# Optimization experiments

Hardware: AMD Instinct MI355X
Metric: run time of the kernel (lower is better)

Reference implementation:

```python
import jax, jax.numpy as jnp
import numpy as np

N = 65536   # nodes
D = 128     # in_dim == emb_dim (required by GRUCell usage)
E = 524288  # edges, pre-sorted by topological level
L = 8       # number of topological levels (edge_masks)


def _gru(x, h, Wi, Wh, bi, bh):
    # torch.nn.GRUCell semantics
    gi = x @ Wi.T + bi            # [*, 3D]
    gh = h @ Wh.T + bh
    ir, iz, i_n = jnp.split(gi, 3, axis=-1)
    hr, hz, h_n = jnp.split(gh, 3, axis=-1)
    r = jax.nn.sigmoid(ir + hr)
    z = jax.nn.sigmoid(iz + hz)
    n = jnp.tanh(i_n + r * h_n)
    return (1.0 - z) * n + z * h


def _direction(h_prev, j_lev, i_lev, ea_lev, We, be, Wa, ba, Wi, Wh, bi, bh):
    # j = message source (h_j gathered), i = aggregation target (segment index)
    n_nodes = h_prev.shape[0]
    # roots = nodes never appearing as aggregation target -> GRU with zero hidden
    root = ~jnp.zeros((n_nodes,), bool).at[i_lev.reshape(-1)].set(True)
    h = jnp.where(root[:, None], _gru(h_prev, jnp.zeros_like(h_prev), Wi, Wh, bi, bh), 0.0)

    def step(h, lev):
        j, i, ea = lev                       # [El], [El], [El, D]
        e = ea @ We.T + be                   # edge_lin
        q = h_prev[i]                        # h_prev_i
        k = h[j] + e                         # h_j + edge_emb
        v = h[j]
        alpha = (jnp.concatenate([q, k], axis=-1) @ Wa.T + ba)[:, 0]  # [El]
        # segment softmax over aggregation index i (numerically stable)
        m = jax.lax.stop_gradient(jax.ops.segment_max(alpha, i, num_segments=n_nodes))
        ex = jnp.exp(alpha - m[i])
        den = jax.ops.segment_sum(ex, i, num_segments=n_nodes)
        a = ex / den[i]
        msg = jax.ops.segment_sum(a[:, None] * v, i, num_segments=n_nodes)  # [N, D]
        mask = jnp.zeros((n_nodes,), bool).at[i].set(True)
        h_new = _gru(h_prev, msg, Wi, Wh, bi, bh)
        return jnp.where(mask[:, None], h_new, h), None

    h, _ = jax.lax.scan(step, h, (j_lev, i_lev, ea_lev))
    return h


def setup_inputs() -> dict:
    key = jax.random.key(0)
    ks = jax.random.split(key, 24)
    p = lambda k, shape: (0.05 * jax.random.normal(k, shape)).astype(jnp.float32)
    inp = {
        'x': jax.random.normal(ks[0], (N, D), jnp.float32),
        'edge_index': jax.random.randint(ks[1], (2, E), 0, N, dtype=jnp.int32),
        'edge_attr': jax.random.normal(ks[2], (E, D), jnp.float32),
        'num_levels': L,
        # forward-direction AttnConv + GRUCell params
        'We_f': p(ks[3], (D, D)), 'be_f': p(ks[4], (D,)),
        'Wa_f': p(ks[5], (1, 2 * D)), 'ba_f': p(ks[6], (1,)),
        'Wi_f': p(ks[7], (3 * D, D)), 'Wh_f': p(ks[8], (3 * D, D)),
        'bi_f': p(ks[9], (3 * D,)), 'bh_f': p(ks[10], (3 * D,)),
        # backward-direction params
        'We_b': p(ks[11], (D, D)), 'be_b': p(ks[12], (D,)),
        'Wa_b': p(ks[13], (1, 2 * D)), 'ba_b': p(ks[14], (1,)),
        'Wi_b': p(ks[15], (3 * D, D)), 'Wh_b': p(ks[16], (3 * D, D)),
        'bi_b': p(ks[17], (3 * D,)), 'bh_b': p(ks[18], (3 * D,)),
    }
    return inp


def reference(x, edge_index, edge_attr, num_levels,
              We_f, be_f, Wa_f, ba_f, Wi_f, Wh_f, bi_f, bh_f,
              We_b, be_b, Wa_b, ba_b, Wi_b, Wh_b, bi_b, bh_b):
    El = edge_index.shape[1] // num_levels
    src = edge_index[0].reshape(num_levels, El)
    dst = edge_index[1].reshape(num_levels, El)
    ea = edge_attr.reshape(num_levels, El, -1)
    # forward pass over levels: flow source->target, aggregate at dst
    h_fwd = _direction(x, src, dst, ea, We_f, be_f, Wa_f, ba_f, Wi_f, Wh_f, bi_f, bh_f)
    # fnb: backward pass takes h_fwd as h_prev; flow target->source (aggregate at src),
    # levels iterated in reverse
    h_bwd = _direction(h_fwd, dst[::-1], src[::-1], ea[::-1],
                       We_b, be_b, Wa_b, ba_b, Wi_b, Wh_b, bi_b, bh_b)
    return jax.nn.relu(h_bwd)
```

## Files before the change

### kernel.cpp

```cpp
#include <hip/hip_runtime.h>
#include <cstdint>
#include <cstddef>

constexpr int N_NODES = 65536;
constexpr int D       = 128;
constexpr int E_EDGES = 524288;
constexpr int LVLS    = 8;
constexpr int EL      = E_EDGES / LVLS;
constexpr int OSTR    = 65540;
constexpr int WIMG_M  = 131072;

typedef unsigned int  u32;
typedef unsigned short u16;
typedef __attribute__((ext_vector_type(8)))  short short8;
typedef __attribute__((ext_vector_type(16))) float f32x16;

__device__ __forceinline__ float sigmoidf_(float x) { return 1.0f / (1.0f + expf(-x)); }

__device__ __forceinline__ u32 bf_hi(float f) {
    u32 x = __float_as_uint(f);
    return (x + 0x7fffu + ((x >> 16) & 1u)) >> 16;
}
__device__ __forceinline__ float bf_f(u32 hbits) { return __uint_as_float(hbits << 16); }

__device__ __forceinline__ int swz(int row, int kbyte) {
    return row * 64 + (kbyte ^ ((row & 3) << 4));
}

__device__ __forceinline__ void gload_lds16(const void* g, void* l) {
    __builtin_amdgcn_global_load_lds(
        (const __attribute__((address_space(1))) unsigned int*)g,
        (__attribute__((address_space(3))) unsigned int*)l, 16, 0, 0);
}

__device__ __forceinline__ float wave_sum(float v) {
#pragma unroll
    for (int off = 32; off > 0; off >>= 1) v += __shfl_down(v, off, 64);
    return v;
}

__global__ __launch_bounds__(256)
void prep_kernel(const float* __restrict__ We_f, const float* __restrict__ Wa_f,
                 const float* __restrict__ be_f, const float* __restrict__ ba_f,
                 const float* __restrict__ We_b, const float* __restrict__ Wa_b,
                 const float* __restrict__ be_b, const float* __restrict__ ba_b,
                 float* __restrict__ u_f, float* __restrict__ u_b, float* __restrict__ cst)
{
    int t = threadIdx.x;
    if (t < 128) {
        float s = 0.f;
        for (int d = 0; d < 128; ++d) s = fmaf(We_f[d * 128 + t], Wa_f[128 + d], s);
        u_f[t] = s;
    } else {
        int c = t - 128;
        float s = 0.f;
        for (int d = 0; d < 128; ++d) s = fmaf(We_b[d * 128 + c], Wa_b[128 + d], s);
        u_b[c] = s;
    }
    if (t == 0) {
        float s = 0.f;
        for (int d = 0; d < 128; ++d) s = fmaf(be_f[d], Wa_f[128 + d], s);
        cst[0] = s + ba_f[0];
    }
    if (t == 255) {
        float s = 0.f;
        for (int d = 0; d < 128; ++d) s = fmaf(be_b[d], Wa_b[128 + d], s);
        cst[1] = s + ba_b[0];
    }
}

__global__ __launch_bounds__(256)
void convert_w4(const float* __restrict__ W0, const float* __restrict__ W1,
                const float* __restrict__ W2, const float* __restrict__ W3,
                unsigned char* __restrict__ img)
{
    const float* Ws[4] = {W0, W1, W2, W3};
    int m = blockIdx.y;
    int i = blockIdx.x * 256 + threadIdx.x;
    int rw = i >> 7, k = i & 127;
    float v = Ws[m][i];
    u32 hb = bf_hi(v);
    u32 lb = bf_hi(v - bf_f(hb));
    int ks = k >> 5, kb = (k & 31) * 2;
    size_t base = (size_t)m * WIMG_M + (size_t)ks * 32768;
    *reinterpret_cast<u16*>(img + base + swz(rw, kb)) = (u16)hb;
    if (rw >= 256)
        *reinterpret_cast<u16*>(img + base + 24576 + swz(rw - 256, kb)) = (u16)lb;
}

__global__ __launch_bounds__(256)
void edot_kernel(const float* __restrict__ ea, const float* __restrict__ u_f,
                 const float* __restrict__ u_b, const float* __restrict__ cst,
                 float* __restrict__ edot_f, float* __restrict__ edot_b)
{
    int wv = threadIdx.x >> 6, lane = threadIdx.x & 63;
    int e = blockIdx.x * 4 + wv;
    if (e >= E_EDGES) return;
    int d = lane << 1;
    float2 v  = *reinterpret_cast<const float2*>(ea + (size_t)e * 128 + d);
    float2 uf = *reinterpret_cast<const float2*>(u_f + d);
    float2 ub = *reinterpret_cast<const float2*>(u_b + d);
    float af = wave_sum(v.x * uf.x + v.y * uf.y);
    float ab = wave_sum(v.x * ub.x + v.y * ub.y);
    if (lane == 0) {
        edot_f[e] = af + cst[0];
        edot_b[e] = ab + cst[1];
    }
}

__global__ __launch_bounds__(256)
void count_flags(const int* __restrict__ ei, int* __restrict__ counts,
                 int* __restrict__ flag_f, int* __restrict__ flag_b)
{
    int e = blockIdx.x * 256 + threadIdx.x;
    int lv = e >> 16;
    int s = ei[e], t = ei[E_EDGES + e];
    atomicAdd(&counts[(size_t)lv * 65536 + t], 1);
    atomicAdd(&counts[(size_t)(8 + lv) * 65536 + s], 1);
    flag_f[t] = 1;
    flag_b[s] = 1;
}

__global__ __launch_bounds__(1024)
void scan_compact(const int* __restrict__ counts, int* __restrict__ offs,
                  int* __restrict__ rows, int* __restrict__ cnts)
{
    __shared__ int sbuf[1024];
    __shared__ int nbuf[1024];
    int dl = blockIdx.x;
    const int4* c4 = reinterpret_cast<const int4*>(counts + (size_t)dl * 65536);
    int* o = offs + (size_t)dl * OSTR;
    int* rw = rows + (size_t)dl * 65536;
    int t = threadIdx.x;
    int cv[64];
#pragma unroll 4
    for (int k4 = 0; k4 < 16; ++k4) {
        int4 v = c4[t * 16 + k4];
        cv[k4 * 4 + 0] = v.x; cv[k4 * 4 + 1] = v.y;
        cv[k4 * 4 + 2] = v.z; cv[k4 * 4 + 3] = v.w;
    }
    int s = 0, nz = 0;
#pragma unroll
    for (int k = 0; k < 64; ++k) { s += cv[k]; nz += (cv[k] > 0); }
    sbuf[t] = s;
    nbuf[t] = nz;
    __syncthreads();
    int val = s, nval = nz;
    for (int off = 1; off < 1024; off <<= 1) {
        int add  = (t >= off) ? sbuf[t - off] : 0;
        int nadd = (t >= off) ? nbuf[t - off] : 0;
        __syncthreads();
        val += add;
        nval += nadd;
        sbuf[t] = val;
        nbuf[t] = nval;
        __syncthreads();
    }
    int run  = val - s;
    int nrun = nval - nz;
    int base = t * 64;
    int4* o4 = reinterpret_cast<int4*>(o + base);
#pragma unroll 4
    for (int k4 = 0; k4 < 16; ++k4) {
        int4 ov;
        ov.x = run; run += cv[k4 * 4 + 0];
        ov.y = run; run += cv[k4 * 4 + 1];
        ov.z = run; run += cv[k4 * 4 + 2];
        ov.w = run; run += cv[k4 * 4 + 3];
        o4[k4] = ov;
#pragma unroll
        for (int q = 0; q < 4; ++q)
            if (cv[k4 * 4 + q] > 0) rw[nrun++] = base + k4 * 4 + q;
    }
    if (t == 1023) { o[65536] = val; cnts[dl] = nval; }
}

__global__ __launch_bounds__(256)
void fill_csr(const int* __restrict__ ei, const float* __restrict__ edot_f,
              const float* __restrict__ edot_b, const int* __restrict__ offs,
              int* __restrict__ cursor, int2* __restrict__ csr)
{
    int idx = blockIdx.x * 256 + threadIdx.x;
    int dir = idx >= E_EDGES;
    int ge = dir ? idx - E_EDGES : idx;
    int lv = ge >> 16;
    int dl = dir * 8 + lv;
    int i = dir ? ei[ge] : ei[E_EDGES + ge];
    int j = dir ? ei[E_EDGES + ge] : ei[ge];
    int pos = offs[(size_t)dl * OSTR + i] + atomicAdd(&cursor[(size_t)dl * 65536 + i], 1);
    int2 v;
    v.x = j;
    v.y = __float_as_int(dir ? edot_b[ge] : edot_f[ge]);
    csr[(size_t)dl * EL + pos] = v;
}

__global__ __launch_bounds__(256)
void root_init(const float* __restrict__ hp, const int* __restrict__ flag,
               const float* __restrict__ Wi, const float* __restrict__ bi,
               const float* __restrict__ bh, const float* __restrict__ wa,
               float* __restrict__ h, float* __restrict__ qdot,
               float* __restrict__ hdot)
{
    int wv = threadIdx.x >> 6, lane = threadIdx.x & 63;
    int n = blockIdx.x * 4 + wv;
    int d = lane << 1;
    const float* hprow = hp + (size_t)n * 128;
    float2 hpv = *reinterpret_cast<const float2*>(hprow + d);
    float qd = wave_sum(hpv.x * wa[d] + hpv.y * wa[d + 1]);
    if (lane == 0) qdot[n] = qd;
    bool root = (flag[n] == 0);
    float hv[2] = {0.f, 0.f};
    if (root) {
#pragma unroll
        for (int q = 0; q < 2; ++q) {
            int dd = d + q;
            float g0 = bi[dd], g1 = bi[dd + 128], g2 = bi[dd + 256];
            for (int k = 0; k < 128; ++k) {
                float a = hprow[k];
                g0 = fmaf(a, Wi[(size_t)dd * 128 + k], g0);
                g1 = fmaf(a, Wi[(size_t)(dd + 128) * 128 + k], g1);
                g2 = fmaf(a, Wi[(size_t)(dd + 256) * 128 + k], g2);
            }
            float rr = sigmoidf_(g0 + bh[dd]);
            float zz = sigmoidf_(g1 + bh[dd + 128]);
            float nn = tanhf(g2 + rr * bh[dd + 256]);
            hv[q] = (1.f - zz) * nn;
        }
        *reinterpret_cast<float2*>(h + (size_t)n * 128 + d) = make_float2(hv[0], hv[1]);
    }
    float hd = wave_sum(hv[0] * wa[128 + d] + hv[1] * wa[128 + d + 1]);
    if (lane == 0) hdot[n] = root ? hd : 0.f;
}

__global__ __launch_bounds__(256)
void attn_msg(const int* __restrict__ pcnt, const int* __restrict__ rows,
              const int* __restrict__ offs, const int2* __restrict__ csr,
              const float* __restrict__ qdot, const float* __restrict__ hdot,
              const float* __restrict__ h, float* __restrict__ msgc)
{
    int cnt = *pcnt;
    int l31 = threadIdx.x & 31;
    int hid = (blockIdx.x * 256 + threadIdx.x) >> 5;
    int nh = (gridDim.x * 256) >> 5;
    int d4 = l31 << 2;
    for (int r = hid; r < cnt; r += nh) {
        int i = rows[r];
        int o0 = offs[i], o1 = offs[i + 1];
        float qi = qdot[i];
        float den = 0.f;
        float4 acc = make_float4(0.f, 0.f, 0.f, 0.f);
        for (int e = o0; e < o1; ++e) {
            int2 je = csr[e];
            float ex = expf(qi + hdot[je.x] + __int_as_float(je.y));
            float4 hv = *reinterpret_cast<const float4*>(h + (size_t)je.x * 128 + d4);
            den += ex;
            acc.x = fmaf(ex, hv.x, acc.x);
            acc.y = fmaf(ex, hv.y, acc.y);
            acc.z = fmaf(ex, hv.z, acc.z);
            acc.w = fmaf(ex, hv.w, acc.w);
        }
        float inv = 1.f / den;
        *reinterpret_cast<float4*>(msgc + (size_t)r * 128 + d4) =
            make_float4(acc.x * inv, acc.y * inv, acc.z * inv, acc.w * inv);
    }
}

__global__ __launch_bounds__(512, 1)
void gemm_gru(const float* __restrict__ msgc, const float* __restrict__ hp,
              const unsigned char* __restrict__ WhImg,
              const unsigned char* __restrict__ WiImg,
              const int* __restrict__ pcnt, const int* __restrict__ rows,
              const float* __restrict__ bi, const float* __restrict__ bh,
              const float* __restrict__ wa,
              float* __restrict__ h, float* __restrict__ hdot)
{
    __shared__ __align__(16) unsigned char smem[16384 + 32768 + 2048 + 512];
    unsigned char* As = smem;
    unsigned char* Bs = smem + 16384;
    float* red   = (float*)(smem + 16384 + 32768);
    int* rowsLds = (int*)(smem + 16384 + 32768 + 2048);

    const int tid = threadIdx.x;
    const int cnt = *pcnt;
    const int row0 = blockIdx.x * 128;
    if (row0 >= cnt) return;

    if (tid < 128) {
        int gr = row0 + tid;
        rowsLds[tid] = (gr < cnt) ? rows[gr] : 0;
    }
    __syncthreads();

    f32x16 acc[2][3];
#pragma unroll
    for (int mt = 0; mt < 2; ++mt)
#pragma unroll
        for (int g = 0; g < 3; ++g) acc[mt][g] = (f32x16)0.0f;
    f32x16 ghn[2];

    const int lane = tid & 63, wv = tid >> 6;
    const int q = wv & 3, mh = wv >> 2;
    const int l31 = lane & 31, l5 = lane >> 5;

#pragma unroll
    for (int ph = 0; ph < 2; ++ph) {
        const float* Asrc = ph ? hp : msgc;
        const unsigned char* Bimg = ph ? WiImg : WhImg;
        for (int ks = 0; ks < 4; ++ks) {
            int k0 = ks * 32;
            {
                const unsigned char* src = Bimg + (size_t)ks * 32768 + wv * 4096 + lane * 16;
                unsigned char* dst = Bs + wv * 4096;
                gload_lds16(src,        dst);
                gload_lds16(src + 1024, dst + 1024);
                gload_lds16(src + 2048, dst + 2048);
                gload_lds16(src + 3072, dst + 3072);
            }
#pragma unroll
            for (int p = 0; p < 2; ++p) {
                int idx = tid + p * 512;
                int rw = idx >> 3, kf = (idx & 7) << 2;
                int arow = ph ? rowsLds[rw] : (row0 + rw);
                float4 v = *reinterpret_cast<const float4*>(Asrc + (size_t)arow * 128 + k0 + kf);
                u32 h0 = bf_hi(v.x), h1 = bf_hi(v.y), h2 = bf_hi(v.z), h3 = bf_hi(v.w);
                u32 l0 = bf_hi(v.x - bf_f(h0)), l1 = bf_hi(v.y - bf_f(h1));
                u32 l2 = bf_hi(v.z - bf_f(h2)), l3 = bf_hi(v.w - bf_f(h3));
                int off = swz(rw, kf * 2);
                *reinterpret_cast<uint2*>(As + off)        = make_uint2(h0 | (h1 << 16), h2 | (h3 << 16));
                *reinterpret_cast<uint2*>(As + 8192 + off) = make_uint2(l0 | (l1 << 16), l2 | (l3 << 16));
            }
            __syncthreads();
#pragma unroll
            for (int kh = 0; kh < 2; ++kh) {
                short8 a[2][2];
#pragma unroll
                for (int mt = 0; mt < 2; ++mt)
#pragma unroll
                    for (int hf = 0; hf < 2; ++hf)
                        a[mt][hf] = *reinterpret_cast<const short8*>(
                            As + hf * 8192 + swz(mh * 64 + mt * 32 + l31, kh * 32 + l5 * 16));
                short8 bh0 = *reinterpret_cast<const short8*>(
                    Bs + swz(q * 32 + l31, kh * 32 + l5 * 16));
                short8 bh1 = *reinterpret_cast<const short8*>(
                    Bs + swz(q * 32 + 128 + l31, kh * 32 + l5 * 16));
                short8 bh2 = *reinterpret_cast<const short8*>(
                    Bs + swz(q * 32 + 256 + l31, kh * 32 + l5 * 16));
                short8 bl2 = *reinterpret_cast<const short8*>(
                    Bs + 24576 + swz(q * 32 + l31, kh * 32 + l5 * 16));
#pragma unroll
                for (int mt = 0; mt < 2; ++mt) {
                    acc[mt][0] = __builtin_amdgcn_mfma_f32_32x32x16_bf16(a[mt][0], bh0, acc[mt][0], 0, 0, 0);
                    acc[mt][0] = __builtin_amdgcn_mfma_f32_32x32x16_bf16(a[mt][1], bh0, acc[mt][0], 0, 0, 0);
                    acc[mt][1] = __builtin_amdgcn_mfma_f32_32x32x16_bf16(a[mt][0], bh1, acc[mt][1], 0, 0, 0);
                    acc[mt][1] = __builtin_amdgcn_mfma_f32_32x32x16_bf16(a[mt][1], bh1, acc[mt][1], 0, 0, 0);
                    acc[mt][2] = __builtin_amdgcn_mfma_f32_32x32x16_bf16(a[mt][0], bh2, acc[mt][2], 0, 0, 0);
                    acc[mt][2] = __builtin_amdgcn_mfma_f32_32x32x16_bf16(a[mt][0], bl2, acc[mt][2], 0, 0, 0);
                    acc[mt][2] = __builtin_amdgcn_mfma_f32_32x32x16_bf16(a[mt][1], bh2, acc[mt][2], 0, 0, 0);
                }
            }
            __syncthreads();
        }
        if (ph == 0) {
            ghn[0] = acc[0][2];
            ghn[1] = acc[1][2];
            acc[0][2] = (f32x16)0.0f;
            acc[1][2] = (f32x16)0.0f;
        }
    }

    const int d = q * 32 + l31;
    const float wa2d = wa[128 + d];
    const float bi0 = bi[d], bi1 = bi[d + 128], bi2 = bi[d + 256];
    const float bh0 = bh[d], bh1 = bh[d + 128], bh2 = bh[d + 256];

#pragma unroll
    for (int mt = 0; mt < 2; ++mt)
#pragma unroll
        for (int rg = 0; rg < 16; ++rg) {
            int rl = mh * 64 + mt * 32 + (rg & 3) + ((rg >> 2) << 3) + (l5 << 2);
            int gr = row0 + rl;
            bool ok = gr < cnt;
            int n = rowsLds[rl];
            float mval = msgc[(size_t)gr * 128 + d];
            float rr = sigmoidf_(acc[mt][0][rg] + bi0 + bh0);
            float zz = sigmoidf_(acc[mt][1][rg] + bi1 + bh1);
            float nn = tanhf(acc[mt][2][rg] + bi2 + rr * (ghn[mt][rg] + bh2));
            float hv = (1.f - zz) * nn + zz * mval;
            if (ok) h[(size_t)n * 128 + d] = hv;
            float pd = hv * wa2d;
#pragma unroll
            for (int o = 1; o < 32; o <<= 1) pd += __shfl_xor(pd, o, 64);
            if (l31 == 0) red[rl * 4 + q] = pd;
        }
    __syncthreads();
    if (tid < 128 && row0 + tid < cnt) {
        int n = rowsLds[tid];
        hdot[n] = red[tid * 4] + red[tid * 4 + 1] + red[tid * 4 + 2] + red[tid * 4 + 3];
    }
}

__global__ __launch_bounds__(256)
void relu_kernel(const float* __restrict__ h, float* __restrict__ out)
{
    int idx = (blockIdx.x * 256 + threadIdx.x) * 4;
    float4 v = *reinterpret_cast<const float4*>(h + idx);
    v.x = fmaxf(v.x, 0.f); v.y = fmaxf(v.y, 0.f);
    v.z = fmaxf(v.z, 0.f); v.w = fmaxf(v.w, 0.f);
    *reinterpret_cast<float4*>(out + idx) = v;
}

extern "C" void kernel_launch(void* const* d_in, const int* in_sizes, int n_in,
                              void* d_out, int out_size, void* d_ws, size_t ws_size,
                              hipStream_t stream)
{
    (void)in_sizes; (void)n_in; (void)out_size; (void)ws_size;

    const float* x    = (const float*)d_in[0];
    const int*   ei   = (const int*)d_in[1];
    const float* ea   = (const float*)d_in[2];
    const float* We_f = (const float*)d_in[4];
    const float* be_f = (const float*)d_in[5];
    const float* Wa_f = (const float*)d_in[6];
    const float* ba_f = (const float*)d_in[7];
    const float* Wi_f = (const float*)d_in[8];
    const float* Wh_f = (const float*)d_in[9];
    const float* bi_f = (const float*)d_in[10];
    const float* bh_f = (const float*)d_in[11];
    const float* We_b = (const float*)d_in[12];
    const float* be_b = (const float*)d_in[13];
    const float* Wa_b = (const float*)d_in[14];
    const float* ba_b = (const float*)d_in[15];
    const float* Wi_b = (const float*)d_in[16];
    const float* Wh_b = (const float*)d_in[17];
    const float* bi_b = (const float*)d_in[18];
    const float* bh_b = (const float*)d_in[19];
    float* out = (float*)d_out;

    char* p = (char*)d_ws;
    auto carve = [&](size_t bytes) -> char* {
        char* r = p;
        p += (bytes + 255) & ~(size_t)255;
        return r;
    };
    int*   counts  = (int*)carve((size_t)16 * 65536 * 4);
    int*   cursor  = (int*)carve((size_t)16 * 65536 * 4);
    int*   flag_f  = (int*)carve((size_t)N_NODES * 4);
    int*   flag_b  = (int*)carve((size_t)N_NODES * 4);
    float* h_fwd   = (float*)carve((size_t)N_NODES * D * 4);
    float* h_cur   = (float*)carve((size_t)N_NODES * D * 4);
    size_t zbytes  = (size_t)((char*)h_cur - (char*)counts) + (size_t)N_NODES * D * 4;
    int*   cnts    = (int*)carve(256);
    unsigned char* Wimg = (unsigned char*)carve((size_t)4 * WIMG_M);
    float* u_f     = (float*)carve((size_t)D * 4);
    float* u_b     = (float*)carve((size_t)D * 4);
    float* cst     = (float*)carve(16);
    float* edot_f  = (float*)carve((size_t)E_EDGES * 4);
    float* edot_b  = (float*)carve((size_t)E_EDGES * 4);
    int*   offs    = (int*)carve((size_t)16 * OSTR * 4);
    int2*  csr     = (int2*)carve((size_t)16 * EL * 8);
    int*   rows    = (int*)carve((size_t)16 * 65536 * 4);
    float* msgc    = (float*)carve((size_t)N_NODES * D * 4);
    float* qdot    = (float*)carve((size_t)N_NODES * 4);
    float* hdot    = (float*)carve((size_t)N_NODES * 4);

    hipMemsetAsync(counts, 0, zbytes, stream);
    prep_kernel<<<1, 256, 0, stream>>>(We_f, Wa_f, be_f, ba_f, We_b, Wa_b, be_b, ba_b,
                                       u_f, u_b, cst);
    convert_w4<<<dim3(192, 4), 256, 0, stream>>>(Wi_f, Wh_f, Wi_b, Wh_b, Wimg);
    count_flags<<<E_EDGES / 256, 256, 0, stream>>>(ei, counts, flag_f, flag_b);
    edot_kernel<<<E_EDGES / 4, 256, 0, stream>>>(ea, u_f, u_b, cst, edot_f, edot_b);
    scan_compact<<<16, 1024, 0, stream>>>(counts, offs, rows, cnts);
    fill_csr<<<2 * E_EDGES / 256, 256, 0, stream>>>(ei, edot_f, edot_b, offs, cursor, csr);

    for (int dir = 0; dir < 2; ++dir) {
        const float* hp   = dir == 0 ? x : h_fwd;
        float*       h    = dir == 0 ? h_fwd : h_cur;
        const unsigned char* WiImg = Wimg + (size_t)(dir * 2) * WIMG_M;
        const unsigned char* WhImg = Wimg + (size_t)(dir * 2 + 1) * WIMG_M;
        const float* Wi   = dir == 0 ? Wi_f : Wi_b;
        const float* bi   = dir == 0 ? bi_f : bi_b;
        const float* bh   = dir == 0 ? bh_f : bh_b;
        const float* wa   = dir == 0 ? Wa_f : Wa_b;
        const int*   flag = dir == 0 ? flag_f : flag_b;

        root_init<<<N_NODES / 4, 256, 0, stream>>>(hp, flag, Wi, bi, bh, wa,
                                                   h, qdot, hdot);

        for (int t = 0; t < LVLS; ++t) {
            int lv = dir == 0 ? t : (LVLS - 1 - t);
            int dl = dir * LVLS + lv;
            attn_msg<<<2048, 256, 0, stream>>>(
                cnts + dl, rows + (size_t)dl * 65536, offs + (size_t)dl * OSTR,
                csr + (size_t)dl * EL, qdot, hdot, h, msgc);
            gemm_gru<<<512, 512, 0, stream>>>(
                msgc, hp, WhImg, WiImg,
                cnts + dl, rows + (size_t)dl * 65536,
                bi, bh, wa, h, hdot);
        }
    }
    relu_kernel<<<(N_NODES * D) / 1024, 256, 0, stream>>>(h_cur, out);
}
```

Measured before the change: 1.683 ms.

## Precompute bf16 hi/lo splits upstream and double-buffer gemm_gru with async LDS loads

Operands are now split into bf16 hi/lo pairs where they are produced (attn_msg, root_init, gemm_gru epilogue, a new convert_x), so gemm_gru no longer converts fp32 to bf16 inside its K loop. The A tiles become direct global-to-LDS loads. The GEMM loop is restructured into an 8-stage double-buffered pipeline with explicit vmcnt waits, overlapping the next stage's loads with the current stage's MFMAs. This costs extra bf16 hi/lo copies of h, msg and x written to global memory, and LDS use doubles to about 100KB.

```diff
diff --git a/kernel.cpp b/kernel.cpp
--- a/kernel.cpp
+++ b/kernel.cpp
@@ -8,7 +8,6 @@
 constexpr int LVLS    = 8;
 constexpr int EL      = E_EDGES / LVLS;
 constexpr int OSTR    = 65540;
-constexpr int WIMG_M  = 131072;
 
 typedef unsigned int  u32;
 typedef unsigned short u16;
@@ -70,9 +69,9 @@
 }
 
 __global__ __launch_bounds__(256)
-void convert_w4(const float* __restrict__ W0, const float* __restrict__ W1,
-                const float* __restrict__ W2, const float* __restrict__ W3,
-                unsigned char* __restrict__ img)
+void convert_w(const float* __restrict__ W0, const float* __restrict__ W1,
+               const float* __restrict__ W2, const float* __restrict__ W3,
+               u16* __restrict__ hi4, u16* __restrict__ lo4)
 {
     const float* Ws[4] = {W0, W1, W2, W3};
     int m = blockIdx.y;
@@ -80,12 +79,23 @@
     int rw = i >> 7, k = i & 127;
     float v = Ws[m][i];
     u32 hb = bf_hi(v);
-    u32 lb = bf_hi(v - bf_f(hb));
-    int ks = k >> 5, kb = (k & 31) * 2;
-    size_t base = (size_t)m * WIMG_M + (size_t)ks * 32768;
-    *reinterpret_cast<u16*>(img + base + swz(rw, kb)) = (u16)hb;
+    hi4[(size_t)m * 49152 + i] = (u16)hb;
     if (rw >= 256)
-        *reinterpret_cast<u16*>(img + base + 24576 + swz(rw - 256, kb)) = (u16)lb;
+        lo4[(size_t)m * 16384 + (size_t)(rw - 256) * 128 + k] = (u16)bf_hi(v - bf_f(hb));
+}
+
+__global__ __launch_bounds__(256)
+void convert_x(const float* __restrict__ x, unsigned char* __restrict__ xhi,
+               unsigned char* __restrict__ xlo)
+{
+    int idx = blockIdx.x * 256 + threadIdx.x;
+    int n = idx >> 6, d = (idx & 63) << 1;
+    float2 v = *reinterpret_cast<const float2*>(x + (size_t)n * 128 + d);
+    u32 h0 = bf_hi(v.x), h1 = bf_hi(v.y);
+    u32 l0 = bf_hi(v.x - bf_f(h0)), l1 = bf_hi(v.y - bf_f(h1));
+    size_t off = (size_t)n * 256 + (size_t)d * 2;
+    *reinterpret_cast<u32*>(xhi + off) = h0 | (h1 << 16);
+    *reinterpret_cast<u32*>(xlo + off) = l0 | (l1 << 16);
 }
 
 __global__ __launch_bounds__(256)
@@ -198,8 +208,9 @@
 void root_init(const float* __restrict__ hp, const int* __restrict__ flag,
                const float* __restrict__ Wi, const float* __restrict__ bi,
                const float* __restrict__ bh, const float* __restrict__ wa,
-               float* __restrict__ h, float* __restrict__ qdot,
-               float* __restrict__ hdot)
+               float* __restrict__ h, unsigned char* __restrict__ h_hi,
+               unsigned char* __restrict__ h_lo,
+               float* __restrict__ qdot, float* __restrict__ hdot)
 {
     int wv = threadIdx.x >> 6, lane = threadIdx.x & 63;
     int n = blockIdx.x * 4 + wv;
@@ -227,6 +238,11 @@
             hv[q] = (1.f - zz) * nn;
         }
         *reinterpret_cast<float2*>(h + (size_t)n * 128 + d) = make_float2(hv[0], hv[1]);
+        u32 hb0 = bf_hi(hv[0]), hb1 = bf_hi(hv[1]);
+        u32 lb0 = bf_hi(hv[0] - bf_f(hb0)), lb1 = bf_hi(hv[1] - bf_f(hb1));
+        size_t off = (size_t)n * 256 + (size_t)d * 2;
+        *reinterpret_cast<u32*>(h_hi + off) = hb0 | (hb1 << 16);
+        *reinterpret_cast<u32*>(h_lo + off) = lb0 | (lb1 << 16);
     }
     float hd = wave_sum(hv[0] * wa[128 + d] + hv[1] * wa[128 + d + 1]);
     if (lane == 0) hdot[n] = root ? hd : 0.f;
@@ -236,7 +252,8 @@
 void attn_msg(const int* __restrict__ pcnt, const int* __restrict__ rows,
               const int* __restrict__ offs, const int2* __restrict__ csr,
               const float* __restrict__ qdot, const float* __restrict__ hdot,
-              const float* __restrict__ h, float* __restrict__ msgc)
+              const float* __restrict__ h, unsigned char* __restrict__ msg_hi,
+              unsigned char* __restrict__ msg_lo)
 {
     int cnt = *pcnt;
     int l31 = threadIdx.x & 31;
@@ -260,25 +277,32 @@
             acc.w = fmaf(ex, hv.w, acc.w);
         }
         float inv = 1.f / den;
-        *reinterpret_cast<float4*>(msgc + (size_t)r * 128 + d4) =
-            make_float4(acc.x * inv, acc.y * inv, acc.z * inv, acc.w * inv);
+        float m0 = acc.x * inv, m1 = acc.y * inv, m2 = acc.z * inv, m3 = acc.w * inv;
+        u32 h0 = bf_hi(m0), h1 = bf_hi(m1), h2 = bf_hi(m2), h3 = bf_hi(m3);
+        u32 l0 = bf_hi(m0 - bf_f(h0)), l1 = bf_hi(m1 - bf_f(h1));
+        u32 l2 = bf_hi(m2 - bf_f(h2)), l3 = bf_hi(m3 - bf_f(h3));
+        size_t off = (size_t)r * 256 + (size_t)d4 * 2;
+        *reinterpret_cast<uint2*>(msg_hi + off) = make_uint2(h0 | (h1 << 16), h2 | (h3 << 16));
+        *reinterpret_cast<uint2*>(msg_lo + off) = make_uint2(l0 | (l1 << 16), l2 | (l3 << 16));
     }
 }
 
 __global__ __launch_bounds__(512, 1)
-void gemm_gru(const float* __restrict__ msgc, const float* __restrict__ hp,
-              const unsigned char* __restrict__ WhImg,
-              const unsigned char* __restrict__ WiImg,
+void gemm_gru(const unsigned char* __restrict__ msg_hi, const unsigned char* __restrict__ msg_lo,
+              const unsigned char* __restrict__ hp_hi, const unsigned char* __restrict__ hp_lo,
+              const u16* __restrict__ Whhi, const u16* __restrict__ Whlo,
+              const u16* __restrict__ Wihi, const u16* __restrict__ Wilo,
               const int* __restrict__ pcnt, const int* __restrict__ rows,
               const float* __restrict__ bi, const float* __restrict__ bh,
               const float* __restrict__ wa,
-              float* __restrict__ h, float* __restrict__ hdot)
-{
-    __shared__ __align__(16) unsigned char smem[16384 + 32768 + 2048 + 512];
+              float* __restrict__ h, unsigned char* __restrict__ h_hi,
+              unsigned char* __restrict__ h_lo, float* __restrict__ hdot)
+{
+    __shared__ __align__(16) unsigned char smem[32768 + 65536 + 2048 + 512];
     unsigned char* As = smem;
-    unsigned char* Bs = smem + 16384;
-    float* red   = (float*)(smem + 16384 + 32768);
-    int* rowsLds = (int*)(smem + 16384 + 32768 + 2048);
+    unsigned char* Bs = smem + 32768;
+    float* red   = (float*)(smem + 98304);
+    int* rowsLds = (int*)(smem + 98304 + 2048);
 
     const int tid = threadIdx.x;
     const int cnt = *pcnt;
@@ -291,81 +315,96 @@
     }
     __syncthreads();
 
-    f32x16 acc[2][3];
-#pragma unroll
-    for (int mt = 0; mt < 2; ++mt)
-#pragma unroll
-        for (int g = 0; g < 3; ++g) acc[mt][g] = (f32x16)0.0f;
-    f32x16 ghn[2];
-
     const int lane = tid & 63, wv = tid >> 6;
     const int q = wv & 3, mh = wv >> 2;
     const int l31 = lane & 31, l5 = lane >> 5;
 
-#pragma unroll
-    for (int ph = 0; ph < 2; ++ph) {
-        const float* Asrc = ph ? hp : msgc;
-        const unsigned char* Bimg = ph ? WiImg : WhImg;
-        for (int ks = 0; ks < 4; ++ks) {
-            int k0 = ks * 32;
-            {
-                const unsigned char* src = Bimg + (size_t)ks * 32768 + wv * 4096 + lane * 16;
-                unsigned char* dst = Bs + wv * 4096;
-                gload_lds16(src,        dst);
-                gload_lds16(src + 1024, dst + 1024);
-                gload_lds16(src + 2048, dst + 2048);
-                gload_lds16(src + 3072, dst + 3072);
+    const int rwA = wv * 16 + (lane >> 2);
+    const int slA = ((lane & 3) << 4) ^ ((rwA & 3) << 4);
+    const size_t baseA0 = (size_t)(row0 + rwA) * 256 + slA;
+    const size_t baseA1 = (size_t)rowsLds[rwA] * 256 + slA;
+    size_t bsrc[3];
+#pragma unroll
+    for (int k = 0; k < 3; ++k) {
+        int rwB = wv * 48 + k * 16 + (lane >> 2);
+        bsrc[k] = (size_t)rwB * 256 + (((lane & 3) << 4) ^ ((rwB & 3) << 4));
+    }
+    const int rwL = wv * 16 + (lane >> 2);
+    const size_t lsrc = (size_t)rwL * 256 + (((lane & 3) << 4) ^ ((rwL & 3) << 4));
+
+    f32x16 acc[2][3];
+#pragma unroll
+    for (int mt = 0; mt < 2; ++mt)
+#pragma unroll
+        for (int g = 0; g < 3; ++g) acc[mt][g] = (f32x16)0.0f;
+    f32x16 ghn[2];
+
+    auto STAGE = [&](int t, int b) {
+        int ph = t >> 2, ks = t & 3;
+        size_t ko = (size_t)ks * 64;
+        const unsigned char* Ahi = ph ? hp_hi : msg_hi;
+        const unsigned char* Alo = ph ? hp_lo : msg_lo;
+        size_t ab = (ph ? baseA1 : baseA0) + ko;
+        unsigned char* Ad = As + b * 16384 + wv * 1024;
+        gload_lds16(Ahi + ab, Ad);
+        gload_lds16(Alo + ab, Ad + 8192);
+        const unsigned char* Bh = (const unsigned char*)(ph ? Wihi : Whhi);
+        const unsigned char* Bl = (const unsigned char*)(ph ? Wilo : Whlo);
+        unsigned char* Bd = Bs + b * 32768;
+#pragma unroll
+        for (int k = 0; k < 3; ++k)
+            gload_lds16(Bh + bsrc[k] + ko, Bd + (wv * 3 + k) * 1024);
+        gload_lds16(Bl + lsrc + ko, Bd + 24576 + wv * 1024);
+    };
+
+    STAGE(0, 0);
+    for (int t = 0; t < 8; ++t) {
+        int b = t & 1;
+        if (t < 7) STAGE(t + 1, b ^ 1);
+        __builtin_amdgcn_sched_barrier(0);
+        if (t < 7) asm volatile("s_waitcnt vmcnt(6)");
+        else       asm volatile("s_waitcnt vmcnt(0)");
+        __builtin_amdgcn_s_barrier();
+        __builtin_amdgcn_sched_barrier(0);
+
+        const unsigned char* Ab = As + b * 16384;
+        const unsigned char* Bb = Bs + b * 32768;
+#pragma unroll
+        for (int kh = 0; kh < 2; ++kh) {
+            short8 a[2][2];
+#pragma unroll
+            for (int mt = 0; mt < 2; ++mt)
+#pragma unroll
+                for (int hf = 0; hf < 2; ++hf)
+                    a[mt][hf] = *reinterpret_cast<const short8*>(
+                        Ab + hf * 8192 + swz(mh * 64 + mt * 32 + l31, kh * 32 + l5 * 16));
+            short8 b0 = *reinterpret_cast<const short8*>(
+                Bb + swz(q * 32 + l31, kh * 32 + l5 * 16));
+            short8 b1 = *reinterpret_cast<const short8*>(
+                Bb + swz(q * 32 + 128 + l31, kh * 32 + l5 * 16));
+            short8 b2 = *reinterpret_cast<const short8*>(
+                Bb + swz(q * 32 + 256 + l31, kh * 32 + l5 * 16));
+            short8 bl2 = *reinterpret_cast<const short8*>(
+                Bb + 24576 + swz(q * 32 + l31, kh * 32 + l5 * 16));
+#pragma unroll
+            for (int mt = 0; mt < 2; ++mt) {
+                acc[mt][0] = __builtin_amdgcn_mfma_f32_32x32x16_bf16(a[mt][0], b0, acc[mt][0], 0, 0, 0);
+                acc[mt][0] = __builtin_amdgcn_mfma_f32_32x32x16_bf16(a[mt][1], b0, acc[mt][0], 0, 0, 0);
+                acc[mt][1] = __builtin_amdgcn_mfma_f32_32x32x16_bf16(a[mt][0], b1, acc[mt][1], 0, 0, 0);
+                acc[mt][1] = __builtin_amdgcn_mfma_f32_32x32x16_bf16(a[mt][1], b1, acc[mt][1], 0, 0, 0);
+                acc[mt][2] = __builtin_amdgcn_mfma_f32_32x32x16_bf16(a[mt][0], b2, acc[mt][2], 0, 0, 0);
+                acc[mt][2] = __builtin_amdgcn_mfma_f32_32x32x16_bf16(a[mt][0], bl2, acc[mt][2], 0, 0, 0);
+                acc[mt][2] = __builtin_amdgcn_mfma_f32_32x32x16_bf16(a[mt][1], b2, acc[mt][2], 0, 0, 0);
             }
-#pragma unroll
-            for (int p = 0; p < 2; ++p) {
-                int idx = tid + p * 512;
-                int rw = idx >> 3, kf = (idx & 7) << 2;
-                int arow = ph ? rowsLds[rw] : (row0 + rw);
-                float4 v = *reinterpret_cast<const float4*>(Asrc + (size_t)arow * 128 + k0 + kf);
-                u32 h0 = bf_hi(v.x), h1 = bf_hi(v.y), h2 = bf_hi(v.z), h3 = bf_hi(v.w);
-                u32 l0 = bf_hi(v.x - bf_f(h0)), l1 = bf_hi(v.y - bf_f(h1));
-                u32 l2 = bf_hi(v.z - bf_f(h2)), l3 = bf_hi(v.w - bf_f(h3));
-                int off = swz(rw, kf * 2);
-                *reinterpret_cast<uint2*>(As + off)        = make_uint2(h0 | (h1 << 16), h2 | (h3 << 16));
-                *reinterpret_cast<uint2*>(As + 8192 + off) = make_uint2(l0 | (l1 << 16), l2 | (l3 << 16));
-            }
-            __syncthreads();
-#pragma unroll
-            for (int kh = 0; kh < 2; ++kh) {
-                short8 a[2][2];
-#pragma unroll
-                for (int mt = 0; mt < 2; ++mt)
-#pragma unroll
-                    for (int hf = 0; hf < 2; ++hf)
-                        a[mt][hf] = *reinterpret_cast<const short8*>(
-                            As + hf * 8192 + swz(mh * 64 + mt * 32 + l31, kh * 32 + l5 * 16));
-                short8 bh0 = *reinterpret_cast<const short8*>(
-                    Bs + swz(q * 32 + l31, kh * 32 + l5 * 16));
-                short8 bh1 = *reinterpret_cast<const short8*>(
-                    Bs + swz(q * 32 + 128 + l31, kh * 32 + l5 * 16));
-                short8 bh2 = *reinterpret_cast<const short8*>(
-                    Bs + swz(q * 32 + 256 + l31, kh * 32 + l5 * 16));
-                short8 bl2 = *reinterpret_cast<const short8*>(
-                    Bs + 24576 + swz(q * 32 + l31, kh * 32 + l5 * 16));
-#pragma unroll
-                for (int mt = 0; mt < 2; ++mt) {
-                    acc[mt][0] = __builtin_amdgcn_mfma_f32_32x32x16_bf16(a[mt][0], bh0, acc[mt][0], 0, 0, 0);
-                    acc[mt][0] = __builtin_amdgcn_mfma_f32_32x32x16_bf16(a[mt][1], bh0, acc[mt][0], 0, 0, 0);
-                    acc[mt][1] = __builtin_amdgcn_mfma_f32_32x32x16_bf16(a[mt][0], bh1, acc[mt][1], 0, 0, 0);
-                    acc[mt][1] = __builtin_amdgcn_mfma_f32_32x32x16_bf16(a[mt][1], bh1, acc[mt][1], 0, 0, 0);
-                    acc[mt][2] = __builtin_amdgcn_mfma_f32_32x32x16_bf16(a[mt][0], bh2, acc[mt][2], 0, 0, 0);
-                    acc[mt][2] = __builtin_amdgcn_mfma_f32_32x32x16_bf16(a[mt][0], bl2, acc[mt][2], 0, 0, 0);
-                    acc[mt][2] = __builtin_amdgcn_mfma_f32_32x32x16_bf16(a[mt][1], bh2, acc[mt][2], 0, 0, 0);
-                }
-            }
-            __syncthreads();
         }
-        if (ph == 0) {
+        if (t == 3) {
             ghn[0] = acc[0][2];
             ghn[1] = acc[1][2];
             acc[0][2] = (f32x16)0.0f;
             acc[1][2] = (f32x16)0.0f;
         }
+        __builtin_amdgcn_s_barrier();
+        __builtin_amdgcn_sched_barrier(0);
     }
 
     const int d = q * 32 + l31;
@@ -381,12 +420,20 @@
             int gr = row0 + rl;
             bool ok = gr < cnt;
             int n = rowsLds[rl];
-            float mval = msgc[(size_t)gr * 128 + d];
+            u16 mhb = *reinterpret_cast<const u16*>(msg_hi + (size_t)gr * 256 + (size_t)d * 2);
+            u16 mlb = *reinterpret_cast<const u16*>(msg_lo + (size_t)gr * 256 + (size_t)d * 2);
+            float mval = bf_f(mhb) + bf_f(mlb);
             float rr = sigmoidf_(acc[mt][0][rg] + bi0 + bh0);
             float zz = sigmoidf_(acc[mt][1][rg] + bi1 + bh1);
             float nn = tanhf(acc[mt][2][rg] + bi2 + rr * (ghn[mt][rg] + bh2));
             float hv = (1.f - zz) * nn + zz * mval;
-            if (ok) h[(size_t)n * 128 + d] = hv;
+            if (ok) {
+                h[(size_t)n * 128 + d] = hv;
+                u32 hb = bf_hi(hv);
+                *reinterpret_cast<u16*>(h_hi + (size_t)n * 256 + (size_t)d * 2) = (u16)hb;
+                *reinterpret_cast<u16*>(h_lo + (size_t)n * 256 + (size_t)d * 2) =
+                    (u16)bf_hi(hv - bf_f(hb));
+            }
             float pd = hv * wa2d;
 #pragma unroll
             for (int o = 1; o < 32; o <<= 1) pd += __shfl_xor(pd, o, 64);
@@ -448,9 +495,18 @@
     int*   flag_b  = (int*)carve((size_t)N_NODES * 4);
     float* h_fwd   = (float*)carve((size_t)N_NODES * D * 4);
     float* h_cur   = (float*)carve((size_t)N_NODES * D * 4);
-    size_t zbytes  = (size_t)((char*)h_cur - (char*)counts) + (size_t)N_NODES * D * 4;
+    unsigned char* hf_hi = (unsigned char*)carve((size_t)N_NODES * 256);
+    unsigned char* hf_lo = (unsigned char*)carve((size_t)N_NODES * 256);
+    size_t zbytes  = (size_t)((char*)hf_lo - (char*)counts) + (size_t)N_NODES * 256;
     int*   cnts    = (int*)carve(256);
-    unsigned char* Wimg = (unsigned char*)carve((size_t)4 * WIMG_M);
+    u16*   Whi4    = (u16*)carve((size_t)4 * 49152 * 2);
+    u16*   Wlo4    = (u16*)carve((size_t)4 * 16384 * 2);
+    unsigned char* x_hi  = (unsigned char*)carve((size_t)N_NODES * 256);
+    unsigned char* x_lo  = (unsigned char*)carve((size_t)N_NODES * 256);
+    unsigned char* hc_hi = (unsigned char*)carve((size_t)N_NODES * 256);
+    unsigned char* hc_lo = (unsigned char*)carve((size_t)N_NODES * 256);
+    unsigned char* msg_hi= (unsigned char*)carve((size_t)N_NODES * 256);
+    unsigned char* msg_lo= (unsigned char*)carve((size_t)N_NODES * 256);
     float* u_f     = (float*)carve((size_t)D * 4);
     float* u_b     = (float*)carve((size_t)D * 4);
     float* cst     = (float*)carve(16);
@@ -459,14 +515,14 @@
     int*   offs    = (int*)carve((size_t)16 * OSTR * 4);
     int2*  csr     = (int2*)carve((size_t)16 * EL * 8);
     int*   rows    = (int*)carve((size_t)16 * 65536 * 4);
-    float* msgc    = (float*)carve((size_t)N_NODES * D * 4);
     float* qdot    = (float*)carve((size_t)N_NODES * 4);
     float* hdot    = (float*)carve((size_t)N_NODES * 4);
 
     hipMemsetAsync(counts, 0, zbytes, stream);
     prep_kernel<<<1, 256, 0, stream>>>(We_f, Wa_f, be_f, ba_f, We_b, Wa_b, be_b, ba_b,
                                        u_f, u_b, cst);
-    convert_w4<<<dim3(192, 4), 256, 0, stream>>>(Wi_f, Wh_f, Wi_b, Wh_b, Wimg);
+    convert_w<<<dim3(192, 4), 256, 0, stream>>>(Wi_f, Wh_f, Wi_b, Wh_b, Whi4, Wlo4);
+    convert_x<<<16384, 256, 0, stream>>>(x, x_hi, x_lo);
     count_flags<<<E_EDGES / 256, 256, 0, stream>>>(ei, counts, flag_f, flag_b);
     edot_kernel<<<E_EDGES / 4, 256, 0, stream>>>(ea, u_f, u_b, cst, edot_f, edot_b);
     scan_compact<<<16, 1024, 0, stream>>>(counts, offs, rows, cnts);
@@ -475,8 +531,14 @@
     for (int dir = 0; dir < 2; ++dir) {
         const float* hp   = dir == 0 ? x : h_fwd;
         float*       h    = dir == 0 ? h_fwd : h_cur;
-        const unsigned char* WiImg = Wimg + (size_t)(dir * 2) * WIMG_M;
-        const unsigned char* WhImg = Wimg + (size_t)(dir * 2 + 1) * WIMG_M;
+        const unsigned char* hp_hi = dir == 0 ? x_hi : hf_hi;
+        const unsigned char* hp_lo = dir == 0 ? x_lo : hf_lo;
+        unsigned char* h_hi = dir == 0 ? hf_hi : hc_hi;
+        unsigned char* h_lo = dir == 0 ? hf_lo : hc_lo;
+        const u16* Wihi = Whi4 + (size_t)(dir * 2) * 49152;
+        const u16* Whhi = Whi4 + (size_t)(dir * 2 + 1) * 49152;
+        const u16* Wilo = Wlo4 + (size_t)(dir * 2) * 16384;
+        const u16* Whlo = Wlo4 + (size_t)(dir * 2 + 1) * 16384;
         const float* Wi   = dir == 0 ? Wi_f : Wi_b;
         const float* bi   = dir == 0 ? bi_f : bi_b;
         const float* bh   = dir == 0 ? bh_f : bh_b;
@@ -484,18 +546,18 @@
         const int*   flag = dir == 0 ? flag_f : flag_b;
 
         root_init<<<N_NODES / 4, 256, 0, stream>>>(hp, flag, Wi, bi, bh, wa,
-                                                   h, qdot, hdot);
+                                                   h, h_hi, h_lo, qdot, hdot);
 
         for (int t = 0; t < LVLS; ++t) {
             int lv = dir == 0 ? t : (LVLS - 1 - t);
             int dl = dir * LVLS + lv;
             attn_msg<<<2048, 256, 0, stream>>>(
                 cnts + dl, rows + (size_t)dl * 65536, offs + (size_t)dl * OSTR,
-                csr + (size_t)dl * EL, qdot, hdot, h, msgc);
+                csr + (size_t)dl * EL, qdot, hdot, h, msg_hi, msg_lo);
             gemm_gru<<<512, 512, 0, stream>>>(
-                msgc, hp, WhImg, WiImg,
+                msg_hi, msg_lo, hp_hi, hp_lo, Whhi, Whlo, Wihi, Wilo,
                 cnts + dl, rows + (size_t)dl * 65536,
-                bi, bh, wa, h, hdot);
+                bi, bh, wa, h, h_hi, h_lo, hdot);
         }
     }
     relu_kernel<<<(N_NODES * D) / 1024, 256, 0, stream>>>(h_cur, out);
```

After: 1.702 ms. About the same (+1.1%).
